# Kernel tuning notes

Measured on AMD Instinct MI355X. Metric: run time of the kernel, lower is better.

Reference implementation:

```python
import jax, jax.numpy as jnp
import numpy as np

B, N, D = 8, 256, 16   # batch, set size, in_dim
HID = 256              # hidden width (hidden_dims[:-1])
H = 128                # attention feature dim (hidden_dims[-1])
DH = 64                # per-dim feature dim d_h
NH = 4                 # attention heads


def _made_masks():
    in_deg = np.arange(1, D + 1)
    h_deg = (np.arange(HID) % (D - 1)) + 1
    out_deg = np.repeat(in_deg, H)  # per-dim contiguous layout -> reshape(..., D, H)
    m0 = h_deg[None, :] >= in_deg[:, None]
    m1 = h_deg[None, :] >= h_deg[:, None]
    m2 = out_deg[None, :] > h_deg[:, None]
    return jnp.array(m0), jnp.array(m1), jnp.array(m2)


def setup_inputs() -> dict:
    key = jax.random.key(0)
    ks = iter(jax.random.split(key, 40))
    def w(fi, fo):
        return jax.random.normal(next(ks), (fi, fo), jnp.float32) / np.sqrt(fi)
    inp = {"t": jnp.array([0.5], jnp.float32),
           "x": jax.random.normal(next(ks), (B, N, D), jnp.float32)}
    qd = [D, HID, HID, H * D]
    kd = [D, HID, HID, H]
    dd = [DH + 2, HID, HID, H, 1]
    for i in range(3):
        inp[f"q_w{i}"] = w(qd[i], qd[i + 1]); inp[f"q_b{i}"] = jnp.zeros((qd[i + 1],), jnp.float32)
        inp[f"k_w{i}"] = w(kd[i], kd[i + 1]); inp[f"k_b{i}"] = jnp.zeros((kd[i + 1],), jnp.float32)
        inp[f"v_w{i}"] = w(kd[i], kd[i + 1]); inp[f"v_b{i}"] = jnp.zeros((kd[i + 1],), jnp.float32)
    inp["p_w"] = w(H, DH); inp["p_b"] = jnp.zeros((DH,), jnp.float32)
    for i in range(4):
        inp[f"d_w{i}"] = w(dd[i], dd[i + 1]); inp[f"d_b{i}"] = jnp.zeros((dd[i + 1],), jnp.float32)
    inp["q_m0"], inp["q_m1"], inp["q_m2"] = _made_masks()
    return inp


def reference(t, x, q_w0, q_b0, k_w0, k_b0, v_w0, v_b0, q_w1, q_b1, k_w1, k_b1, v_w1, v_b1,
              q_w2, q_b2, k_w2, k_b2, v_w2, v_b2, p_w, p_b,
              d_w0, d_b0, d_w1, d_b1, d_w2, d_b2, d_w3, d_b3, q_m0, q_m1, q_m2):
    # --- exclusive net: MADE query (hollow per dim), MLP key/value, diagonal-masked attention ---
    hq = jax.nn.relu(x @ (q_w0 * q_m0) + q_b0)
    hq = jax.nn.relu(hq @ (q_w1 * q_m1) + q_b1)
    q = (hq @ (q_w2 * q_m2) + q_b2).reshape(B, N, D, H)      # [B,N,D,H]

    def mlp3(z, w0, b0, w1, b1, w2, b2):
        z = jnp.tanh(z @ w0 + b0)
        z = jnp.tanh(z @ w1 + b1)
        return z @ w2 + b2

    k = mlp3(x, k_w0, k_b0, k_w1, k_b1, k_w2, k_b2)          # [B,N,H] (shared across dims)
    v = mlp3(x, v_w0, v_b0, v_w1, v_b1, v_w2, v_b2)          # [B,N,H]

    dh = H // NH
    qh = q.transpose(0, 2, 1, 3).reshape(B, D, N, NH, dh).transpose(0, 1, 3, 2, 4)  # [B,D,NH,N,dh]
    kh = k.reshape(B, N, NH, dh).transpose(0, 2, 1, 3)        # [B,NH,N,dh]
    vh = v.reshape(B, N, NH, dh).transpose(0, 2, 1, 3)

    # einsum avoids materializing the repeat_interleaved key/value (same math)
    scores = jnp.einsum('bdhnc,bhmc->bdhnm', qh, kh) / np.sqrt(dh)
    scores = jnp.where(jnp.eye(N, dtype=bool), -jnp.inf, scores)  # mask self-attention (hollow)
    att = jax.nn.softmax(scores, axis=-1)
    o = jnp.einsum('bdhnm,bhmc->bdhnc', att, vh)              # [B,D,NH,N,dh]
    o = o.transpose(0, 1, 3, 2, 4).reshape(B, D, N, H).transpose(0, 2, 1, 3)  # [B,N,D,H]
    hfeat = o @ p_w + p_b                                     # [B,N,D,DH], hollow wrt x[...,d]

    # --- dimwise net: y_d = MLP([t, x_d, h_d]); exact diagonal Jacobian via jvp on x channel ---
    tb = jnp.broadcast_to(t.reshape(()), (B, N, D, 1)).astype(x.dtype)
    def dimwise(xc):
        z = jnp.concatenate([tb, xc, hfeat], -1)              # [B,N,D,2+DH]
        z = jnp.tanh(z @ d_w0 + d_b0)
        z = jnp.tanh(z @ d_w1 + d_b1)
        z = jnp.tanh(z @ d_w2 + d_b2)
        return (z @ d_w3 + d_b3)[..., 0]                      # [B,N,D]

    y, jac = jax.jvp(dimwise, (x[..., None],), (jnp.ones((B, N, D, 1), x.dtype),))
    return y, jac
```

## Files before the change

kernel.cpp:

```cpp
#include <hip/hip_runtime.h>
#include <hip/hip_bf16.h>

constexpr int kB = 8, kN = 256, kD = 16, kHID = 256, kH = 128, kDH = 64, kdh = 32;
constexpr int kBN = kB * kN;
constexpr int kP  = kBN * kD;

__device__ __forceinline__ float b2f(__hip_bfloat16 v) { return __bfloat162float(v); }
__device__ __forceinline__ __hip_bfloat16 f2b(float v) { return __float2bfloat16(v); }
__device__ __forceinline__ unsigned short f2bs(float v) {
    __hip_bfloat16 h = __float2bfloat16(v);
    return *(unsigned short*)&h;
}

__device__ __forceinline__ float tanh_fast(float v) {
    float e = __expf(2.f * v);
    return 1.f - 2.f * __builtin_amdgcn_rcpf(e + 1.f);
}

typedef short s8v  __attribute__((ext_vector_type(8)));
typedef float f4v  __attribute__((ext_vector_type(4)));
#define MFMA(a, b, c) __builtin_amdgcn_mfma_f32_16x16x32_bf16((a), (b), (c), 0, 0, 0)

struct KParams {
    const float *t, *x;
    const float *q_b0, *k_b0, *v_b0, *q_b1, *k_b1, *v_b1, *k_b2, *v_b2, *q_b2;
    const float *p_w, *p_b;
    const float *d_w0, *d_b0, *d_b1, *d_b2, *d_w3, *d_b3, *d_w1, *d_w2;
    const float *k_w0, *k_w1, *k_w2, *v_w0, *v_w1, *v_w2, *q_w0, *q_w1, *q_w2;
    __hip_bfloat16 *pwf, *w0f, *w1f, *w2f;
    __hip_bfloat16 *k0f, *k1f, *k2f, *v0f, *v1f, *v2f, *q0f, *q1f, *q2f;
    __hip_bfloat16 *kbufF, *vbufF, *h1qF, *obuf;
    float *out;
};

__device__ __forceinline__ void prep_tile(const KParams& P, int tile, int lane)
{
    const float* src; __hip_bfloat16* dst; int N, NT, local, Kreal = 1 << 30, mask = 0;
    if (tile < 16)        { src = P.p_w;        dst = P.pwf; N = 64;   NT = 4;   local = tile; }
    else if (tile < 48)   { src = P.d_w0 + 512; dst = P.w0f; N = 256;  NT = 16;  local = tile - 16; }
    else if (tile < 176)  { src = P.d_w1;       dst = P.w1f; N = 256;  NT = 16;  local = tile - 48; }
    else if (tile < 240)  { src = P.d_w2;       dst = P.w2f; N = 128;  NT = 8;   local = tile - 176; }
    else if (tile < 256)  { src = P.k_w0;       dst = P.k0f; N = 256;  NT = 16;  local = tile - 240; Kreal = 16; }
    else if (tile < 272)  { src = P.v_w0;       dst = P.v0f; N = 256;  NT = 16;  local = tile - 256; Kreal = 16; }
    else if (tile < 288)  { src = P.q_w0;       dst = P.q0f; N = 256;  NT = 16;  local = tile - 272; Kreal = 16; mask = 1; }
    else if (tile < 416)  { src = P.k_w1;       dst = P.k1f; N = 256;  NT = 16;  local = tile - 288; }
    else if (tile < 544)  { src = P.v_w1;       dst = P.v1f; N = 256;  NT = 16;  local = tile - 416; }
    else if (tile < 672)  { src = P.q_w1;       dst = P.q1f; N = 256;  NT = 16;  local = tile - 544; mask = 2; }
    else if (tile < 736)  { src = P.k_w2;       dst = P.k2f; N = 128;  NT = 8;   local = tile - 672; }
    else if (tile < 800)  { src = P.v_w2;       dst = P.v2f; N = 128;  NT = 8;   local = tile - 736; }
    else                  { src = P.q_w2;       dst = P.q2f; N = 2048; NT = 128; local = tile - 800; mask = 3; }
    const int kt = local / NT, nt = local % NT;
    const int row0 = kt * 32 + (lane >> 4) * 8;
    const int col  = nt * 16 + (lane & 15);
    __hip_bfloat16* o = dst + ((size_t)local * 64 + lane) * 8;
    #pragma unroll
    for (int j = 0; j < 8; ++j) {
        const int r = row0 + j;
        float w = (r < Kreal) ? src[(size_t)r * N + col] : 0.f;
        if (mask == 1 && !((col % 15) >= r))        w = 0.f;
        if (mask == 2 && !((col % 15) >= (r % 15))) w = 0.f;
        if (mask == 3 && !((col >> 7) > (r % 15)))  w = 0.f;
        o[j] = f2b(w);
    }
}

__global__ __launch_bounds__(256) void prep_mlpw_kernel(KParams P)
{
    const int s = blockIdx.x * 4 + (threadIdx.x >> 6);
    prep_tile(P, 240 + s, threadIdx.x & 63);
}

__global__ __launch_bounds__(256) void mlp_kernel(KParams P)
{
    constexpr int SA = 264;
    constexpr int SX = 40;
    __shared__ __hip_bfloat16 xin[32 * SX];
    __shared__ __hip_bfloat16 bufA[32 * SA];
    __shared__ __hip_bfloat16 bufB[32 * SA];

    const int tid  = threadIdx.x;
    const int wv   = tid >> 6, lane = tid & 63;

    if (blockIdx.x >= 192) {
        const int s = (blockIdx.x - 192) * 4 + wv;
        prep_tile(P, 800 + s, lane);
        return;
    }

    const int lx   = lane & 15, quad = lane >> 4;
    const int path = blockIdx.x >> 6;
    const int r0   = (blockIdx.x & 63) * 32;

    auto ldA = [&](const __hip_bfloat16* buf, int stride, int m0, int k0) -> s8v {
        return *(const s8v*)(buf + (m0 + lx) * stride + k0 + quad * 8);
    };
    auto ldB = [&](const __hip_bfloat16* wf, int NT, int kt, int nt) -> s8v {
        return *(const s8v*)(wf + (((size_t)(kt * NT + nt) * 64 + lane) << 3));
    };

    for (int idx = tid; idx < 1024; idx += 256) {
        const int row = idx >> 5, c = idx & 31;
        xin[row * SX + c] = f2b(c < 16 ? P.x[(r0 + row) * kD + c] : 0.f);
    }

    const __hip_bfloat16* F0[3] = { P.k0f, P.v0f, P.q0f };
    const __hip_bfloat16* F1[3] = { P.k1f, P.v1f, P.q1f };
    const __hip_bfloat16* F2[2] = { P.k2f, P.v2f };
    const float* Ba0[3] = { P.k_b0, P.v_b0, P.q_b0 };
    const float* Ba1[3] = { P.k_b1, P.v_b1, P.q_b1 };
    const float* Ba2[2] = { P.k_b2, P.v_b2 };

    __syncthreads();

    {
        f4v acc[4][2] = {};
        const s8v a0 = ldA(xin, SX, 0, 0);
        const s8v a1 = ldA(xin, SX, 16, 0);
        #pragma unroll
        for (int j = 0; j < 4; ++j) {
            s8v b = ldB(F0[path], 16, 0, wv * 4 + j);
            acc[j][0] = MFMA(a0, b, acc[j][0]);
            acc[j][1] = MFMA(a1, b, acc[j][1]);
        }
        #pragma unroll
        for (int j = 0; j < 4; ++j) {
            const int n = (wv * 4 + j) * 16 + lx;
            const float bb = Ba0[path][n];
            #pragma unroll
            for (int mt = 0; mt < 2; ++mt)
            #pragma unroll
            for (int r = 0; r < 4; ++r) {
                const float v = acc[j][mt][r] + bb;
                const float z = (path == 2) ? fmaxf(v, 0.f) : tanh_fast(v);
                bufA[(mt * 16 + quad * 4 + r) * SA + n] = f2b(z);
            }
        }
    }
    __syncthreads();

    {
        f4v acc[4][2] = {};
        #pragma unroll
        for (int kt = 0; kt < 8; ++kt) {
            const s8v a0 = ldA(bufA, SA, 0, kt * 32);
            const s8v a1 = ldA(bufA, SA, 16, kt * 32);
            #pragma unroll
            for (int j = 0; j < 4; ++j) {
                s8v b = ldB(F1[path], 16, kt, wv * 4 + j);
                acc[j][0] = MFMA(a0, b, acc[j][0]);
                acc[j][1] = MFMA(a1, b, acc[j][1]);
            }
        }
        #pragma unroll
        for (int j = 0; j < 4; ++j) {
            const int n = (wv * 4 + j) * 16 + lx;
            const float bb = Ba1[path][n];
            #pragma unroll
            for (int mt = 0; mt < 2; ++mt)
            #pragma unroll
            for (int r = 0; r < 4; ++r) {
                const int m = mt * 16 + quad * 4 + r;
                const float v = acc[j][mt][r] + bb;
                if (path == 2) {
                    const int kt2 = (wv * 4 + j) >> 1;
                    const int q2  = ((wv * 4 + j) & 1) * 2 + (lx >> 3);
                    P.h1qF[(size_t)(((r0 >> 4) + mt) * 8 + kt2) * 512
                         + (q2 * 16 + quad * 4 + r) * 8 + (lx & 7)] = f2b(fmaxf(v, 0.f));
                } else {
                    bufB[m * SA + n] = f2b(tanh_fast(v));
                }
            }
        }
    }
    if (path == 2) return;
    __syncthreads();

    {
        f4v acc[2][2] = {};
        #pragma unroll
        for (int kt = 0; kt < 8; ++kt) {
            const s8v a0 = ldA(bufB, SA, 0, kt * 32);
            const s8v a1 = ldA(bufB, SA, 16, kt * 32);
            #pragma unroll
            for (int j = 0; j < 2; ++j) {
                s8v b = ldB(F2[path], 8, kt, wv * 2 + j);
                acc[j][0] = MFMA(a0, b, acc[j][0]);
                acc[j][1] = MFMA(a1, b, acc[j][1]);
            }
        }
        const int bidx = r0 >> 8;
        const int ktv  = (r0 >> 5) & 7;
        #pragma unroll
        for (int j = 0; j < 2; ++j) {
            const int n  = (wv * 2 + j) * 16 + lx;
            const float bb = Ba2[path][n];
            const int hd = n >> 5;
            #pragma unroll
            for (int mt = 0; mt < 2; ++mt)
            #pragma unroll
            for (int r = 0; r < 4; ++r) {
                const int gr = r0 + mt * 16 + quad * 4 + r;
                const __hip_bfloat16 hv = f2b(acc[j][mt][r] + bb);
                if (path == 0) {
                    const int mtg = (gr >> 4) & 15;
                    P.kbufF[(size_t)(((bidx * 4 + hd) * 16 + mtg) * 64
                          + ((n & 31) >> 3) * 16 + (gr & 15)) * 8 + (lx & 7)] = hv;
                } else {
                    const int m5 = gr & 31;
                    P.vbufF[(size_t)((((bidx * 4 + hd) * 2 + ((n >> 4) & 1)) * 8 + ktv) * 64
                          + (m5 >> 3) * 16 + lx) * 8 + (m5 & 7)] = hv;
                }
            }
        }
    }
}

__global__ __launch_bounds__(256, 2) void attn_kernel(KParams P)
{
    constexpr int SP = 264;
    constexpr int QP = 40;
    __shared__ short Pl[4][16 * SP];
    __shared__ short Qw[256 * QP];

    const int wv   = threadIdx.x >> 6;
    const int lane = threadIdx.x & 63;

    if (blockIdx.x >= 512) {
        const int s = (blockIdx.x - 512) * 4 + wv;
        prep_tile(P, s, lane);
        return;
    }

    const int blk = blockIdx.x;
    const int hd = blk & 3;
    const int d  = (blk >> 2) & 15;
    const int b  = blk >> 6;

    const int lx = lane & 15, quad = lane >> 4;
    short* Pw = &Pl[wv][0];

    const short* hq = (const short*)P.h1qF;
    const short* kb = (const short*)P.kbufF;
    const short* vb = (const short*)P.vbufF;
    const int bh = b * 4 + hd;

    f4v qacc[4][2] = {};
    #pragma unroll
    for (int kt = 0; kt < 8; ++kt) {
        const s8v b0 = *(const s8v*)(P.q2f + (((size_t)(kt * 128 + d * 8 + hd * 2 + 0) * 64 + lane) << 3));
        const s8v b1 = *(const s8v*)(P.q2f + (((size_t)(kt * 128 + d * 8 + hd * 2 + 1) * 64 + lane) << 3));
        #pragma unroll
        for (int mt = 0; mt < 4; ++mt) {
            const s8v a = *(const s8v*)(hq + ((size_t)((b * 16 + wv * 4 + mt) * 8 + kt) * 512 + lane * 8));
            qacc[mt][0] = MFMA(a, b0, qacc[mt][0]);
            qacc[mt][1] = MFMA(a, b1, qacc[mt][1]);
        }
    }

    s8v kfrag[16];
    #pragma unroll
    for (int mt = 0; mt < 16; ++mt)
        kfrag[mt] = *(const s8v*)(kb + ((size_t)(bh * 16 + mt) * 64 + lane) * 8);
    s8v vfrag[2][8];
    #pragma unroll
    for (int ntv = 0; ntv < 2; ++ntv)
    #pragma unroll
    for (int kt = 0; kt < 8; ++kt)
        vfrag[ntv][kt] = *(const s8v*)(vb + ((size_t)((bh * 2 + ntv) * 8 + kt) * 64 + lane) * 8);

    {
        const float scale = 0.17677669529663687f;
        #pragma unroll
        for (int jn = 0; jn < 2; ++jn) {
            const float bb = P.q_b2[d * 128 + hd * 32 + jn * 16 + lx];
            #pragma unroll
            for (int mt = 0; mt < 4; ++mt)
            #pragma unroll
            for (int r = 0; r < 4; ++r) {
                const int lrow = wv * 64 + mt * 16 + quad * 4 + r;
                Qw[lrow * QP + jn * 16 + lx] = (short)f2bs((qacc[mt][jn][r] + bb) * scale);
            }
        }
    }
    __syncthreads();

    const float LOG2E = 1.4426950408889634f;

    for (int mi = 0; mi < 4; ++mi) {
        const int q0 = wv * 64 + mi * 16;

        const s8v qfrag = *(const s8v*)(Qw + (q0 + lx) * QP + quad * 8);

        f4v acc[16];
        #pragma unroll
        for (int mt = 0; mt < 16; ++mt) acc[mt] = f4v{0.f, 0.f, 0.f, 0.f};
        #pragma unroll
        for (int mt = 0; mt < 16; ++mt) acc[mt] = MFMA(kfrag[mt], qfrag, acc[mt]);

        const int qg = q0 + lx;
        float mx = -3.0e38f;
        #pragma unroll
        for (int mt = 0; mt < 16; ++mt)
        #pragma unroll
        for (int r = 0; r < 4; ++r) {
            const int key = mt * 16 + quad * 4 + r;
            float s = (key == qg) ? -3.0e38f : acc[mt][r];
            acc[mt][r] = s;
            mx = fmaxf(mx, s);
        }
        mx = fmaxf(mx, __shfl_xor(mx, 16, 64));
        mx = fmaxf(mx, __shfl_xor(mx, 32, 64));

        const float nmxc = -mx * LOG2E;
        float l = 0.f;
        #pragma unroll
        for (int mt = 0; mt < 16; ++mt)
        #pragma unroll
        for (int r = 0; r < 4; ++r) {
            float p = exp2f(__builtin_fmaf(acc[mt][r], LOG2E, nmxc));
            acc[mt][r] = p;
            l += p;
        }
        l += __shfl_xor(l, 16, 64);
        l += __shfl_xor(l, 32, 64);

        #pragma unroll
        for (int mt = 0; mt < 16; ++mt) {
            unsigned short h0 = f2bs(acc[mt][0]);
            unsigned short h1 = f2bs(acc[mt][1]);
            unsigned short h2 = f2bs(acc[mt][2]);
            unsigned short h3 = f2bs(acc[mt][3]);
            uint2 w;
            w.x = (unsigned int)h0 | ((unsigned int)h1 << 16);
            w.y = (unsigned int)h2 | ((unsigned int)h3 << 16);
            *(uint2*)(Pw + lx * SP + mt * 16 + quad * 4) = w;
        }
        __asm__ volatile("s_waitcnt lgkmcnt(0)" ::: "memory");

        f4v av[2] = { f4v{0.f,0.f,0.f,0.f}, f4v{0.f,0.f,0.f,0.f} };
        #pragma unroll
        for (int kt = 0; kt < 8; ++kt) {
            s8v a = *(const s8v*)(Pw + lx * SP + kt * 32 + quad * 8);
            av[0] = MFMA(a, vfrag[0][kt], av[0]);
            av[1] = MFMA(a, vfrag[1][kt], av[1]);
        }
        __asm__ volatile("s_waitcnt lgkmcnt(0)" ::: "memory");

        #pragma unroll
        for (int r = 0; r < 4; ++r) {
            const float lr = __shfl(l, quad * 4 + r, 64);
            const float inv = __builtin_amdgcn_rcpf(lr);
            const int qrow = q0 + quad * 4 + r;
            #pragma unroll
            for (int ntv = 0; ntv < 2; ++ntv) {
                P.obuf[((size_t)((b * 256 + qrow) * 16 + d)) * 128 + hd * 32 + ntv * 16 + lx]
                    = f2b(av[ntv][r] * inv);
            }
        }
    }
}

__global__ __launch_bounds__(256, 2) void dim_kernel(KParams P)
{
    constexpr int SA = 264;
    constexpr int SO = 136;
    constexpr int SH = 72;
    __shared__ __hip_bfloat16 bufA[64 * SA];
    __shared__ __hip_bfloat16 bufB[64 * SA];
    __shared__ __hip_bfloat16 bufH[32 * SH];
    __shared__ float xvs[32];

    const int tid  = threadIdx.x;
    const int wv   = tid >> 6, lane = tid & 63;
    const int lx   = lane & 15, quad = lane >> 4;
    const int p0   = blockIdx.x * 32;
    const float tval = P.t[0];

    auto ldA = [&](const __hip_bfloat16* buf, int stride, int m0, int k0) -> s8v {
        return *(const s8v*)(buf + (m0 + lx) * stride + k0 + quad * 8);
    };
    auto ldBf = [&](const __hip_bfloat16* wf, int NT, int kt, int nt) -> s8v {
        return *(const s8v*)(wf + (((size_t)(kt * NT + nt) * 64 + lane) << 3));
    };

    for (int idx = tid; idx < 512; idx += 256) {
        const int row = idx >> 4, ch = idx & 15;
        *(f4v*)(bufA + row * SO + ch * 8) = *(const f4v*)(P.obuf + (size_t)(p0 + row) * kH + ch * 8);
    }
    if (tid < 32) xvs[tid] = P.x[p0 + tid];
    __syncthreads();

    {
        f4v acc0 = {}, acc1 = {};
        #pragma unroll
        for (int ktile = 0; ktile < 4; ++ktile) {
            s8v b  = ldBf(P.pwf, 4, ktile, wv);
            s8v a0 = ldA(bufA, SO, 0,  ktile * 32);
            s8v a1 = ldA(bufA, SO, 16, ktile * 32);
            acc0 = MFMA(a0, b, acc0);
            acc1 = MFMA(a1, b, acc1);
        }
        const int n = wv * 16 + lx;
        const float bb = P.p_b[n];
        #pragma unroll
        for (int r = 0; r < 4; ++r) {
            bufH[(quad * 4 + r) * SH + n]        = f2b(acc0[r] + bb);
            bufH[(quad * 4 + r + 16) * SH + n]   = f2b(acc1[r] + bb);
        }
    }
    __syncthreads();

    {
        f4v acc[4][2] = {};
        #pragma unroll
        for (int ktile = 0; ktile < 2; ++ktile) {
            s8v a0 = ldA(bufH, SH, 0,  ktile * 32);
            s8v a1 = ldA(bufH, SH, 16, ktile * 32);
            #pragma unroll
            for (int j = 0; j < 4; ++j) {
                s8v b = ldBf(P.w0f, 16, ktile, wv * 4 + j);
                acc[j][0] = MFMA(a0, b, acc[j][0]);
                acc[j][1] = MFMA(a1, b, acc[j][1]);
            }
        }
        #pragma unroll
        for (int j = 0; j < 4; ++j) {
            const int n = (wv * 4 + j) * 16 + lx;
            const float base = P.d_b0[n] + tval * P.d_w0[n];
            const float wx   = P.d_w0[256 + n];
            #pragma unroll
            for (int mt = 0; mt < 2; ++mt)
            #pragma unroll
            for (int r = 0; r < 4; ++r) {
                const int m = mt * 16 + quad * 4 + r;
                const float z = tanh_fast(acc[j][mt][r] + base + xvs[m] * wx);
                bufB[m * SA + n]        = f2b(z);
                bufB[(m + 32) * SA + n] = f2b((1.f - z * z) * wx);
            }
        }
    }
    __syncthreads();

    {
        f4v acc[4][4] = {};
        #pragma unroll
        for (int ktile = 0; ktile < 8; ++ktile) {
            s8v a0 = ldA(bufB, SA, 0,  ktile * 32);
            s8v a1 = ldA(bufB, SA, 16, ktile * 32);
            s8v a2 = ldA(bufB, SA, 32, ktile * 32);
            s8v a3 = ldA(bufB, SA, 48, ktile * 32);
            #pragma unroll
            for (int j = 0; j < 4; ++j) {
                s8v b = ldBf(P.w1f, 16, ktile, wv * 4 + j);
                acc[j][0] = MFMA(a0, b, acc[j][0]);
                acc[j][1] = MFMA(a1, b, acc[j][1]);
                acc[j][2] = MFMA(a2, b, acc[j][2]);
                acc[j][3] = MFMA(a3, b, acc[j][3]);
            }
        }
        #pragma unroll
        for (int j = 0; j < 4; ++j) {
            const int n = (wv * 4 + j) * 16 + lx;
            const float b1 = P.d_b1[n];
            #pragma unroll
            for (int mt = 0; mt < 2; ++mt)
            #pragma unroll
            for (int r = 0; r < 4; ++r) {
                const int m = mt * 16 + quad * 4 + r;
                const float z  = tanh_fast(acc[j][mt][r] + b1);
                const float zd = (1.f - z * z) * acc[j][mt + 2][r];
                bufA[m * SA + n]        = f2b(z);
                bufA[(m + 32) * SA + n] = f2b(zd);
            }
        }
    }
    __syncthreads();

    {
        f4v acc[2][4] = {};
        #pragma unroll
        for (int ktile = 0; ktile < 8; ++ktile) {
            s8v a0 = ldA(bufA, SA, 0,  ktile * 32);
            s8v a1 = ldA(bufA, SA, 16, ktile * 32);
            s8v a2 = ldA(bufA, SA, 32, ktile * 32);
            s8v a3 = ldA(bufA, SA, 48, ktile * 32);
            #pragma unroll
            for (int j = 0; j < 2; ++j) {
                s8v b = ldBf(P.w2f, 8, ktile, wv * 2 + j);
                acc[j][0] = MFMA(a0, b, acc[j][0]);
                acc[j][1] = MFMA(a1, b, acc[j][1]);
                acc[j][2] = MFMA(a2, b, acc[j][2]);
                acc[j][3] = MFMA(a3, b, acc[j][3]);
            }
        }
        #pragma unroll
        for (int j = 0; j < 2; ++j) {
            const int n = (wv * 2 + j) * 16 + lx;
            const float b2 = P.d_b2[n];
            #pragma unroll
            for (int mt = 0; mt < 2; ++mt)
            #pragma unroll
            for (int r = 0; r < 4; ++r) {
                const int m = mt * 16 + quad * 4 + r;
                const float z  = tanh_fast(acc[j][mt][r] + b2);
                const float zd = (1.f - z * z) * acc[j][mt + 2][r];
                bufB[m * SO + n]        = f2b(z);
                bufB[(m + 32) * SO + n] = f2b(zd);
            }
        }
    }
    __syncthreads();

    {
        const int p = tid >> 3, s = tid & 7;
        float yv = 0.f, jv = 0.f;
        #pragma unroll
        for (int i = 0; i < 16; ++i) {
            const int n = s + i * 8;
            const float w = P.d_w3[n];
            yv += b2f(bufB[p * SO + n]) * w;
            jv += b2f(bufB[(p + 32) * SO + n]) * w;
        }
        #pragma unroll
        for (int off = 4; off > 0; off >>= 1) {
            yv += __shfl_down(yv, off, 8);
            jv += __shfl_down(jv, off, 8);
        }
        if (s == 0) {
            P.out[p0 + p]      = yv + P.d_b3[0];
            P.out[kP + p0 + p] = jv;
        }
    }
}

extern "C" void kernel_launch(void* const* d_in, const int* in_sizes, int n_in,
                              void* d_out, int out_size, void* d_ws, size_t ws_size,
                              hipStream_t stream)
{
    typedef const float* fp;
    KParams P;
    P.t    = (fp)d_in[0];
    P.x    = (fp)d_in[1];
    P.q_w0 = (fp)d_in[2];  P.q_b0 = (fp)d_in[3];
    P.k_w0 = (fp)d_in[4];  P.k_b0 = (fp)d_in[5];
    P.v_w0 = (fp)d_in[6];  P.v_b0 = (fp)d_in[7];
    P.q_w1 = (fp)d_in[8];  P.q_b1 = (fp)d_in[9];
    P.k_w1 = (fp)d_in[10]; P.k_b1 = (fp)d_in[11];
    P.v_w1 = (fp)d_in[12]; P.v_b1 = (fp)d_in[13];
    P.q_w2 = (fp)d_in[14]; P.q_b2 = (fp)d_in[15];
    P.k_w2 = (fp)d_in[16]; P.k_b2 = (fp)d_in[17];
    P.v_w2 = (fp)d_in[18]; P.v_b2 = (fp)d_in[19];
    P.p_w  = (fp)d_in[20]; P.p_b  = (fp)d_in[21];
    P.d_w0 = (fp)d_in[22]; P.d_b0 = (fp)d_in[23];
    P.d_w1 = (fp)d_in[24]; P.d_b1 = (fp)d_in[25];
    P.d_w2 = (fp)d_in[26]; P.d_b2 = (fp)d_in[27];
    P.d_w3 = (fp)d_in[28]; P.d_b3 = (fp)d_in[29];

    __hip_bfloat16* wsb = (__hip_bfloat16*)d_ws;
    P.kbufF = wsb;
    P.vbufF = P.kbufF + (size_t)kBN * kH;
    P.obuf  = P.vbufF + (size_t)kBN * kH;
    P.pwf   = P.obuf + (size_t)kP * kH;
    P.w0f   = P.pwf + 8192;
    P.w1f   = P.w0f + 16384;
    P.w2f   = P.w1f + 65536;
    P.k0f   = P.w2f + 32768;
    P.v0f   = P.k0f + 8192;
    P.q0f   = P.v0f + 8192;
    P.k1f   = P.q0f + 8192;
    P.v1f   = P.k1f + 65536;
    P.q1f   = P.v1f + 65536;
    P.k2f   = P.q1f + 65536;
    P.v2f   = P.k2f + 32768;
    P.q2f   = P.v2f + 32768;
    P.h1qF  = P.q2f + 524288;
    P.out   = (float*)d_out;

    prep_mlpw_kernel<<<140, 256, 0, stream>>>(P);
    mlp_kernel<<<448, 256, 0, stream>>>(P);
    attn_kernel<<<572, 256, 0, stream>>>(P);
    dim_kernel<<<kP / 32, 256, 0, stream>>>(P);
}
```

Measured before the change: 192.4 us.

## Fuse prep, MLP, attention and dimwise kernels into one persistent kernel with grid barriers

Merges the four separate launches into a single 512-block persistent kernel whose stages are separated by atomic-counter grid barriers. A small init kernel resets the counters first. Weight-prep tiles are redistributed across the idle blocks in the first two stages, and each block runs two dimwise tiles from one shared-memory arena. The goal is to cut inter-kernel launch gaps and drain time. The cost is barrier spin overhead, and correctness now depends on all 512 blocks being resident at once; the spin loop has a timeout fallback that could break ordering.

```diff
diff --git a/kernel.cpp b/kernel.cpp
--- a/kernel.cpp
+++ b/kernel.cpp
@@ -30,8 +30,28 @@
     __hip_bfloat16 *pwf, *w0f, *w1f, *w2f;
     __hip_bfloat16 *k0f, *k1f, *k2f, *v0f, *v1f, *v2f, *q0f, *q1f, *q2f;
     __hip_bfloat16 *kbufF, *vbufF, *h1qF, *obuf;
+    unsigned *bar;
     float *out;
 };
+
+constexpr unsigned kGrid = 512;
+
+__device__ __forceinline__ void gbar(unsigned* bar, int idx)
+{
+    __syncthreads();
+    if (threadIdx.x == 0) {
+        __threadfence();
+        __hip_atomic_fetch_add(&bar[idx], 1u, __ATOMIC_ACQ_REL, __HIP_MEMORY_SCOPE_AGENT);
+        unsigned v; long spins = 0;
+        do {
+            v = __hip_atomic_load(&bar[idx], __ATOMIC_ACQUIRE, __HIP_MEMORY_SCOPE_AGENT);
+            if (++spins > 5000000) break;
+            if (v < kGrid) __builtin_amdgcn_s_sleep(2);
+        } while (v < kGrid);
+        __threadfence();
+    }
+    __syncthreads();
+}
 
 __device__ __forceinline__ void prep_tile(const KParams& P, int tile, int lane)
 {
@@ -64,32 +84,19 @@
     }
 }
 
-__global__ __launch_bounds__(256) void prep_mlpw_kernel(KParams P)
-{
-    const int s = blockIdx.x * 4 + (threadIdx.x >> 6);
-    prep_tile(P, 240 + s, threadIdx.x & 63);
-}
-
-__global__ __launch_bounds__(256) void mlp_kernel(KParams P)
+__device__ __forceinline__ void mlp_body(const KParams& P, char* smem, int blk)
 {
     constexpr int SA = 264;
     constexpr int SX = 40;
-    __shared__ __hip_bfloat16 xin[32 * SX];
-    __shared__ __hip_bfloat16 bufA[32 * SA];
-    __shared__ __hip_bfloat16 bufB[32 * SA];
+    __hip_bfloat16* xin  = (__hip_bfloat16*)smem;
+    __hip_bfloat16* bufA = (__hip_bfloat16*)(smem + 2560);
+    __hip_bfloat16* bufB = (__hip_bfloat16*)(smem + 19456);
 
     const int tid  = threadIdx.x;
     const int wv   = tid >> 6, lane = tid & 63;
-
-    if (blockIdx.x >= 192) {
-        const int s = (blockIdx.x - 192) * 4 + wv;
-        prep_tile(P, 800 + s, lane);
-        return;
-    }
-
     const int lx   = lane & 15, quad = lane >> 4;
-    const int path = blockIdx.x >> 6;
-    const int r0   = (blockIdx.x & 63) * 32;
+    const int path = blk >> 6;
+    const int r0   = (blk & 63) * 32;
 
     auto ldA = [&](const __hip_bfloat16* buf, int stride, int m0, int k0) -> s8v {
         return *(const s8v*)(buf + (m0 + lx) * stride + k0 + quad * 8);
@@ -215,29 +222,21 @@
     }
 }
 
-__global__ __launch_bounds__(256, 2) void attn_kernel(KParams P)
+__device__ __forceinline__ void attn_body(const KParams& P, char* smem, int blk)
 {
     constexpr int SP = 264;
     constexpr int QP = 40;
-    __shared__ short Pl[4][16 * SP];
-    __shared__ short Qw[256 * QP];
-
-    const int wv   = threadIdx.x >> 6;
-    const int lane = threadIdx.x & 63;
-
-    if (blockIdx.x >= 512) {
-        const int s = (blockIdx.x - 512) * 4 + wv;
-        prep_tile(P, s, lane);
-        return;
-    }
-
-    const int blk = blockIdx.x;
+    short* Pl = (short*)smem;
+    short* Qw = (short*)(smem + 33792);
+
     const int hd = blk & 3;
     const int d  = (blk >> 2) & 15;
     const int b  = blk >> 6;
 
+    const int wv   = threadIdx.x >> 6;
+    const int lane = threadIdx.x & 63;
     const int lx = lane & 15, quad = lane >> 4;
-    short* Pw = &Pl[wv][0];
+    short* Pw = Pl + wv * 16 * SP;
 
     const short* hq = (const short*)P.h1qF;
     const short* kb = (const short*)P.kbufF;
@@ -360,20 +359,20 @@
     }
 }
 
-__global__ __launch_bounds__(256, 2) void dim_kernel(KParams P)
+__device__ __forceinline__ void dim_body(const KParams& P, char* smem, int tile)
 {
     constexpr int SA = 264;
     constexpr int SO = 136;
     constexpr int SH = 72;
-    __shared__ __hip_bfloat16 bufA[64 * SA];
-    __shared__ __hip_bfloat16 bufB[64 * SA];
-    __shared__ __hip_bfloat16 bufH[32 * SH];
-    __shared__ float xvs[32];
+    __hip_bfloat16* bufA = (__hip_bfloat16*)smem;
+    __hip_bfloat16* bufB = (__hip_bfloat16*)(smem + 33792);
+    __hip_bfloat16* bufH = (__hip_bfloat16*)(smem + 67584);
+    float* xvs = (float*)(smem + 72192);
 
     const int tid  = threadIdx.x;
     const int wv   = tid >> 6, lane = tid & 63;
     const int lx   = lane & 15, quad = lane >> 4;
-    const int p0   = blockIdx.x * 32;
+    const int p0   = tile * 32;
     const float tval = P.t[0];
 
     auto ldA = [&](const __hip_bfloat16* buf, int stride, int m0, int k0) -> s8v {
@@ -404,8 +403,8 @@
         const float bb = P.p_b[n];
         #pragma unroll
         for (int r = 0; r < 4; ++r) {
-            bufH[(quad * 4 + r) * SH + n]        = f2b(acc0[r] + bb);
-            bufH[(quad * 4 + r + 16) * SH + n]   = f2b(acc1[r] + bb);
+            bufH[(quad * 4 + r) * SH + n]      = f2b(acc0[r] + bb);
+            bufH[(quad * 4 + r + 16) * SH + n] = f2b(acc1[r] + bb);
         }
     }
     __syncthreads();
@@ -531,6 +530,41 @@
             P.out[kP + p0 + p] = jv;
         }
     }
+}
+
+__global__ __launch_bounds__(64) void init_kernel(KParams P)
+{
+    if (threadIdx.x < 8) P.bar[threadIdx.x] = 0u;
+    __threadfence();
+}
+
+__global__ __launch_bounds__(256, 2) void fused_kernel(KParams P)
+{
+    __shared__ __align__(16) char smem[72448];
+    const int wv   = threadIdx.x >> 6;
+    const int lane = threadIdx.x & 63;
+    const int blk  = blockIdx.x;
+
+    {
+        const int s = blk * 4 + wv;
+        if (s < 560) prep_tile(P, 240 + s, lane);
+    }
+    gbar(P.bar, 0);
+
+    if (blk < 192) {
+        mlp_body(P, smem, blk);
+    } else {
+        const int s = (blk - 192) * 4 + wv;
+        if (s < 1264) prep_tile(P, (s < 240) ? s : 560 + s, lane);
+    }
+    gbar(P.bar, 1);
+
+    attn_body(P, smem, blk);
+    gbar(P.bar, 2);
+
+    dim_body(P, smem, blk * 2 + 0);
+    __syncthreads();
+    dim_body(P, smem, blk * 2 + 1);
 }
 
 extern "C" void kernel_launch(void* const* d_in, const int* in_sizes, int n_in,
@@ -574,10 +608,9 @@
     P.v2f   = P.k2f + 32768;
     P.q2f   = P.v2f + 32768;
     P.h1qF  = P.q2f + 524288;
+    P.bar   = (unsigned*)((char*)d_ws + (size_t)(32 << 20));
     P.out   = (float*)d_out;
 
-    prep_mlpw_kernel<<<140, 256, 0, stream>>>(P);
-    mlp_kernel<<<448, 256, 0, stream>>>(P);
-    attn_kernel<<<572, 256, 0, stream>>>(P);
-    dim_kernel<<<kP / 32, 256, 0, stream>>>(P);
-}
+    init_kernel<<<1, 64, 0, stream>>>(P);
+    fused_kernel<<<kGrid, 256, 0, stream>>>(P);
+}
```

Measured after the change: 433.6 us. 2.25x slower.
